# Optimization experiments

Hardware: AMD Instinct MI355X
Metric: run time of the kernel (lower is better)

Reference implementation:

```python
import jax, jax.numpy as jnp
import numpy as np

SIGMA = 1.0
DELTA = 1.0
TOPK = 10
TOPK_HALF = int(np.around(TOPK / 2))  # 5
EPS = 1e-12


def _cdist(a, b):
    # Euclidean distance matrix, grad-safe sqrt at zero (matches torch.cdist values).
    d2 = (jnp.sum(a * a, axis=1)[:, None]
          + jnp.sum(b * b, axis=1)[None, :]
          - 2.0 * (a @ b.T))
    d2 = jnp.maximum(d2, 0.0)
    pos = d2 > 0.0
    return jnp.where(pos, jnp.sqrt(jnp.where(pos, d2, 1.0)), 0.0)


def _consistency_weights(t_emb):
    # Everything here is under torch.no_grad() in the original.
    N = t_emb.shape[0]
    T_dist = _cdist(t_emb, t_emb)
    W_P = jnp.exp(-(T_dist ** 2) / SIGMA)
    _, idx = jax.lax.top_k(W_P, TOPK)                      # [N, TOPK]
    rows = jnp.arange(N)[:, None]
    W_NN = jnp.zeros_like(W_P).at[rows, idx].set(1.0)      # scatter_ ones
    V = (((W_NN + W_NN.T) / 2) == 1.0).astype(W_P.dtype)   # mutual kNN (symmetric)
    # Vectorized form of the per-row python loop:
    #   W_C_tilda[i, j] = V[i, j] * (sum_k V[i, k] * V[j, k]) / sum_k V[i, k]
    deg = jnp.sum(V, axis=1)                               # >= 1 (self is always a NN)
    overlap = V @ V.T                                      # [N, N] neighbor overlap
    W_C_tilda = V * overlap / deg[:, None]
    topk_half_index = idx[:, :TOPK_HALF]                   # [N, TOPK_HALF]
    W_C_hat = jnp.mean(W_C_tilda[topk_half_index], axis=1) # gather rows, mean -> [N, N]
    W_C = (W_C_hat + W_C_hat.T) / 2
    return (W_P + W_C) / 2


def reference(s_emb, t_emb):
    # disable_mu = 0 -> s_emb NOT normalized; t_emb always normalized.
    t_norm = t_emb / jnp.maximum(
        jnp.linalg.norm(t_emb, axis=1, keepdims=True), EPS)
    N = s_emb.shape[0]
    S_dist = _cdist(s_emb, s_emb)
    S_dist = S_dist / jnp.mean(S_dist, axis=1, keepdims=True)
    W = jax.lax.stop_gradient(_consistency_weights(t_norm))
    off_diag = 1.0 - jnp.eye(N, dtype=W.dtype)
    pos_weight = W * off_diag
    neg_weight = (1.0 - W) * off_diag
    pull = jnp.maximum(S_dist, 0.0) ** 2 * pos_weight
    push = jnp.maximum(DELTA - S_dist, 0.0) ** 2 * neg_weight
    return (jnp.sum(pull) + jnp.sum(push)) / (N * (N - 1))


def setup_inputs() -> dict:
    key = jax.random.key(0)
    k1, k2 = jax.random.split(key)
    N, D = 2048, 1024
    return {
        "s_emb": jax.random.normal(k1, (N, D), dtype=jnp.float32),
        "t_emb": jax.random.normal(k2, (N, D), dtype=jnp.float32),
    }
```

## Files before the change

### kernel.cpp

```cpp
#include <hip/hip_runtime.h>
#include <math.h>

#define N_ 2048
#define D_ 1024
#define TOPK 10
#define TOPK_HALF 5
#define INV_NORM (1.0f / ((float)N_ * (float)(N_ - 1)))

typedef __attribute__((ext_vector_type(8))) short short8;
typedef __attribute__((ext_vector_type(4))) float floatx4;

__device__ __forceinline__ short f2bf(float f) {
  unsigned u = __float_as_uint(f);
  unsigned r = (u + 0x7fffu + ((u >> 16) & 1u)) >> 16;
  return (short)r;
}
__device__ __forceinline__ float bf2f(short b) {
  return __uint_as_float(((unsigned)(unsigned short)b) << 16);
}

__device__ __forceinline__ void gld_lds16(const short* g, short* l) {
  __builtin_amdgcn_global_load_lds(
      (const __attribute__((address_space(1))) unsigned int*)(g),
      (__attribute__((address_space(3))) unsigned int*)(l), 16, 0, 0);
}

#define BAR() asm volatile("s_barrier" ::: "memory")
#define WAIT8_BAR() asm volatile("s_waitcnt vmcnt(8)\ns_barrier" ::: "memory")
#define WAIT0_BAR() asm volatile("s_waitcnt vmcnt(0)\ns_barrier" ::: "memory")

__global__ __launch_bounds__(256) void prep_kernel(const float* __restrict__ t,
                                                   const float* __restrict__ s,
                                                   short* __restrict__ tb,
                                                   short* __restrict__ sb,
                                                   float* __restrict__ tt,
                                                   float* __restrict__ ss,
                                                   float* __restrict__ rowsum,
                                                   float* __restrict__ out) {
  int b = blockIdx.x, tid = threadIdx.x;
  __shared__ float red[256];
  if (b == 0) {
    for (int j = tid; j < N_; j += 256) rowsum[j] = 0.f;
    if (tid == 0) out[0] = 0.f;
  }
  if (b < N_) {
    const float* rp = t + (size_t)b * D_;
    short* op = tb + (size_t)b * D_;
    float acc = 0.f;
    for (int k = tid; k < D_; k += 256) { float v = rp[k]; acc += v * v; }
    red[tid] = acc; __syncthreads();
    for (int st = 128; st > 0; st >>= 1) { if (tid < st) red[tid] += red[tid + st]; __syncthreads(); }
    float denom = fmaxf(sqrtf(red[0]), 1e-12f);
    __syncthreads();
    float s2 = 0.f;
    for (int k = tid; k < D_; k += 256) { float v = rp[k] / denom; op[k] = f2bf(v); s2 += v * v; }
    red[tid] = s2; __syncthreads();
    for (int st = 128; st > 0; st >>= 1) { if (tid < st) red[tid] += red[tid + st]; __syncthreads(); }
    if (tid == 0) tt[b] = red[0];
  } else {
    int row = b - N_;
    const float* rp = s + (size_t)row * D_;
    short* op = sb + (size_t)row * D_;
    float acc = 0.f;
    for (int k = tid; k < D_; k += 256) { float v = rp[k]; op[k] = f2bf(v); acc += v * v; }
    red[tid] = acc; __syncthreads();
    for (int st = 128; st > 0; st >>= 1) { if (tid < st) red[tid] += red[tid + st]; __syncthreads(); }
    if (tid == 0) ss[row] = red[0];
  }
}

__global__ __launch_bounds__(256) void gram_mfma_kernel(
    const short* __restrict__ Tb, const short* __restrict__ Sb,
    const float* __restrict__ tt, const float* __restrict__ ss,
    short* __restrict__ WPb, short* __restrict__ Sob,
    float* __restrict__ rowsum) {
  const int mode = blockIdx.z;
  const short* A = mode ? Sb : Tb;
  const float* rn = mode ? ss : tt;
  short* outb = mode ? Sob : WPb;

  __shared__ __align__(16) short As[2][128 * 64];
  __shared__ __align__(16) short Bs[2][128 * 64];

  int tid = threadIdx.x;
  int w = tid >> 6, lane = tid & 63;
  int i0 = blockIdx.y * 128, j0 = blockIdx.x * 128;
  int wr = w >> 1, wc = w & 1;
  int quad = lane >> 4, l16 = lane & 15;

  floatx4 acc[4][4] = {};

  int srow = w * 32 + (lane >> 3);
  int gchunk = ((lane & 7) ^ (lane >> 3)) * 8;
  const short* Ag = A + (size_t)(i0 + srow) * D_ + gchunk;
  const short* Bg = A + (size_t)(j0 + srow) * D_ + gchunk;
  int sloc = srow * 64 + (lane & 7) * 8;

#define STAGE(buf, k0)                                        \
  do {                                                        \
    _Pragma("unroll") for (int q = 0; q < 4; q++) {           \
      gld_lds16(Ag + (k0) + (size_t)q * 8 * D_, &As[buf][sloc + q * 8 * 64]); \
      gld_lds16(Bg + (k0) + (size_t)q * 8 * D_, &Bs[buf][sloc + q * 8 * 64]); \
    }                                                         \
  } while (0)

  STAGE(0, 0);
#pragma unroll 2
  for (int it = 0; it < 16; it++) {
    int cur = it & 1;
    if (it) BAR();
    if (it < 15) {
      STAGE(!cur, (it + 1) * 64);
      WAIT8_BAR();
    } else {
      WAIT0_BAR();
    }
    const short* Ab = As[cur];
    const short* Bb = Bs[cur];
#pragma unroll
    for (int ks = 0; ks < 64; ks += 32) {
      int cb = ks >> 3;
      short8 af[4], bfr[4];
#pragma unroll
      for (int mt = 0; mt < 4; mt++) {
        int r = wr * 64 + mt * 16 + l16;
        af[mt] = *(const short8*)&Ab[r * 64 + (((cb + quad) ^ (l16 & 7)) << 3)];
      }
#pragma unroll
      for (int nt = 0; nt < 4; nt++) {
        int r = wc * 64 + nt * 16 + l16;
        bfr[nt] = *(const short8*)&Bb[r * 64 + (((cb + quad) ^ (l16 & 7)) << 3)];
      }
#pragma unroll
      for (int mt = 0; mt < 4; mt++)
#pragma unroll
        for (int nt = 0; nt < 4; nt++)
          acc[mt][nt] = __builtin_amdgcn_mfma_f32_16x16x32_bf16(af[mt], bfr[nt], acc[mt][nt], 0, 0, 0);
    }
  }

#pragma unroll
  for (int mt = 0; mt < 4; mt++) {
#pragma unroll
    for (int r = 0; r < 4; r++) {
      int i = i0 + wr * 64 + mt * 16 + quad * 4 + r;
      float ri = rn[i];
      float rs = 0.f;
#pragma unroll
      for (int nt = 0; nt < 4; nt++) {
        int j = j0 + wc * 64 + nt * 16 + l16;
        float d2 = fmaxf(ri + rn[j] - 2.f * acc[mt][nt][r], 0.f);
        float o = mode ? sqrtf(d2) : expf(-d2);
        if (i == j) o = mode ? 0.f : 1.f;
        outb[(size_t)i * N_ + j] = f2bf(o);
        rs += o;
      }
      if (mode) {
        rs += __shfl_xor(rs, 1); rs += __shfl_xor(rs, 2);
        rs += __shfl_xor(rs, 4); rs += __shfl_xor(rs, 8);
        if (l16 == 0) atomicAdd(&rowsum[i], rs);
      }
    }
  }
}

__global__ __launch_bounds__(64) void topk_loss_kernel(const short* __restrict__ WPb,
                                                       const short* __restrict__ Sb,
                                                       const float* __restrict__ rowsum,
                                                       int* __restrict__ idx,
                                                       unsigned* __restrict__ mask,
                                                       float* __restrict__ out) {
  int row = blockIdx.x, lane = threadIdx.x;
  const short8* wpr = (const short8*)(WPb + (size_t)row * N_);
  const short8* sr = (const short8*)(Sb + (size_t)row * N_);
  float rminv = (float)N_ / rowsum[row];
  float w[32];
  float local = 0.f;
#pragma unroll
  for (int c4 = 0; c4 < 4; c4++) {
    short8 wp8 = wpr[lane * 4 + c4];
    short8 s8 = sr[lane * 4 + c4];
#pragma unroll
    for (int e = 0; e < 8; e++) {
      float wv = bf2f(wp8[e]);
      w[c4 * 8 + e] = wv;
      float sv = bf2f(s8[e]) * rminv;
      float d = fmaxf(1.f - sv, 0.f);
      local += d * d + 0.5f * wv * (sv * sv - d * d);
    }
  }
#pragma unroll
  for (int off = 32; off > 0; off >>= 1) local += __shfl_down(local, off);
  if (lane == 0) {
    atomicAdd(out, (local - 0.5f) * INV_NORM);
    mask[row] = 0u;
  }
  int base = lane * 32;
  int sel[TOPK];
  for (int t = 0; t < TOPK; t++) {
    float bv = -2.f; int bi = 0;
#pragma unroll
    for (int c = 0; c < 32; c++)
      if (w[c] > bv) { bv = w[c]; bi = base + c; }
#pragma unroll
    for (int off = 32; off > 0; off >>= 1) {
      float ov = __shfl_down(bv, off);
      int oi = __shfl_down(bi, off);
      if (ov > bv || (ov == bv && oi < bi)) { bv = ov; bi = oi; }
    }
    bi = __shfl(bi, 0);
    sel[t] = bi;
    bool mine = (bi >> 5) == lane;
    int cc = bi & 31;
#pragma unroll
    for (int c = 0; c < 32; c++)
      if (mine && cc == c) w[c] = -1.f;
  }
  if (lane == 0) {
#pragma unroll
    for (int t = 0; t < TOPK; t++) idx[row * TOPK + t] = sel[t];
  }
}

__global__ __launch_bounds__(256) void mutual_kernel(const int* __restrict__ idx,
                                                     unsigned* __restrict__ mask) {
  int t = blockIdx.x * 256 + threadIdx.x;
  int i = t >> 4, k = t & 15;
  if (i >= N_ || k >= TOPK) return;
  int j = idx[i * TOPK + k];
  bool mut = false;
#pragma unroll
  for (int l = 0; l < TOPK; l++) mut |= (idx[j * TOPK + l] == i);
  if (mut) atomicOr(&mask[i], 1u << k);
}

__global__ __launch_bounds__(256) void sparse_wc_kernel(
    const int* __restrict__ idx, const unsigned* __restrict__ mask,
    const short* __restrict__ Sb, const float* __restrict__ rowsum,
    float* __restrict__ out) {
  int t = blockIdx.x * 256 + threadIdx.x;
  int i = t >> 6, r = t & 63;
  float contrib = 0.f;
  if (i < N_ && r < TOPK_HALF * TOPK) {
    int mi = r / TOPK, k = r - mi * TOPK;
    int m = idx[i * TOPK + mi];
    unsigned mm = mask[m];
    if ((mm >> k) & 1u) {
      int col = idx[m * TOPK + k];
      if (col != i) {
        int dm = __popc(mm);
        unsigned mc = mask[col];
        int jm[TOPK], jc[TOPK];
#pragma unroll
        for (int l = 0; l < TOPK; l++) jm[l] = idx[m * TOPK + l];
#pragma unroll
        for (int l = 0; l < TOPK; l++) jc[l] = idx[col * TOPK + l];
        int c = 0;
#pragma unroll
        for (int a = 0; a < TOPK; a++) {
          if ((mm >> a) & 1u) {
            int na = jm[a];
#pragma unroll
            for (int b = 0; b < TOPK; b++) c += (((mc >> b) & 1u) && (jc[b] == na));
          }
        }
        float v = (float)c / (float)dm * 0.1f;
        float s1 = bf2f(Sb[(size_t)i * N_ + col]) * ((float)N_ / rowsum[i]);
        float d1 = fmaxf(1.f - s1, 0.f);
        float s2 = bf2f(Sb[(size_t)col * N_ + i]) * ((float)N_ / rowsum[col]);
        float d2 = fmaxf(1.f - s2, 0.f);
        contrib = 0.5f * v * ((s1 * s1 - d1 * d1) + (s2 * s2 - d2 * d2));
      }
    }
  }
  __shared__ float red[256];
  red[threadIdx.x] = contrib; __syncthreads();
  for (int st = 128; st > 0; st >>= 1) {
    if (threadIdx.x < st) red[threadIdx.x] += red[threadIdx.x + st];
    __syncthreads();
  }
  if (threadIdx.x == 0) atomicAdd(out, red[0] * INV_NORM);
}

extern "C" void kernel_launch(void* const* d_in, const int* in_sizes, int n_in,
                              void* d_out, int out_size, void* d_ws, size_t ws_size,
                              hipStream_t stream) {
  const float* s_emb = (const float*)d_in[0];
  const float* t_emb = (const float*)d_in[1];
  float* out = (float*)d_out;

  const size_t NN = (size_t)N_ * N_;
  const size_t ND = (size_t)N_ * D_;
  short* t_bf = (short*)d_ws;
  short* s_bf = t_bf + ND;
  short* WPb = s_bf + ND;
  short* Sb = WPb + NN;
  float* tt = (float*)(Sb + NN);
  float* ss = tt + N_;
  float* rowsum = ss + N_;
  int* idx = (int*)(rowsum + N_);
  unsigned* mask = (unsigned*)(idx + (size_t)N_ * TOPK);

  prep_kernel<<<2 * N_, 256, 0, stream>>>(t_emb, s_emb, t_bf, s_bf, tt, ss, rowsum, out);

  dim3 g(N_ / 128, N_ / 128, 2);
  gram_mfma_kernel<<<g, 256, 0, stream>>>(t_bf, s_bf, tt, ss, WPb, Sb, rowsum);

  topk_loss_kernel<<<N_, 64, 0, stream>>>(WPb, Sb, rowsum, idx, mask, out);
  mutual_kernel<<<N_ * 16 / 256, 256, 0, stream>>>(idx, mask);
  sparse_wc_kernel<<<N_ * 64 / 256, 256, 0, stream>>>(idx, mask, Sb, rowsum, out);
}
```

Baseline: 149.7 us.

## Exploit Gram symmetry with 64x64 triangular tiles and vectorize prep kernel

The Gram kernel now computes only lower-triangular 64x64 tiles (528 per matrix) and writes each off-diagonal tile's transpose through LDS, also adding column sums to rowsum for the S distance matrix. This roughly halves the MFMA work, at the cost of smaller tiles with less register reuse, extra transposed stores and more atomics. The prep kernel is rewritten to load each row once as float4 and store packed bf16 pairs, removing the second global read of t.

```diff
diff --git a/kernel.cpp b/kernel.cpp
--- a/kernel.cpp
+++ b/kernel.cpp
@@ -26,7 +26,7 @@
 }
 
 #define BAR() asm volatile("s_barrier" ::: "memory")
-#define WAIT8_BAR() asm volatile("s_waitcnt vmcnt(8)\ns_barrier" ::: "memory")
+#define WAIT4_BAR() asm volatile("s_waitcnt vmcnt(4)\ns_barrier" ::: "memory")
 #define WAIT0_BAR() asm volatile("s_waitcnt vmcnt(0)\ns_barrier" ::: "memory")
 
 __global__ __launch_bounds__(256) void prep_kernel(const float* __restrict__ t,
@@ -44,64 +44,80 @@
     if (tid == 0) out[0] = 0.f;
   }
   if (b < N_) {
-    const float* rp = t + (size_t)b * D_;
-    short* op = tb + (size_t)b * D_;
-    float acc = 0.f;
-    for (int k = tid; k < D_; k += 256) { float v = rp[k]; acc += v * v; }
-    red[tid] = acc; __syncthreads();
+    const float4* rp = (const float4*)(t + (size_t)b * D_);
+    float4 v = rp[tid];
+    red[tid] = v.x * v.x + v.y * v.y + v.z * v.z + v.w * v.w;
+    __syncthreads();
     for (int st = 128; st > 0; st >>= 1) { if (tid < st) red[tid] += red[tid + st]; __syncthreads(); }
-    float denom = fmaxf(sqrtf(red[0]), 1e-12f);
-    __syncthreads();
-    float s2 = 0.f;
-    for (int k = tid; k < D_; k += 256) { float v = rp[k] / denom; op[k] = f2bf(v); s2 += v * v; }
-    red[tid] = s2; __syncthreads();
+    float inv = 1.f / fmaxf(sqrtf(red[0]), 1e-12f);
+    __syncthreads();
+    float a = v.x * inv, bb = v.y * inv, c = v.z * inv, d = v.w * inv;
+    uint2 pk;
+    pk.x = (unsigned)(unsigned short)f2bf(a) | ((unsigned)(unsigned short)f2bf(bb) << 16);
+    pk.y = (unsigned)(unsigned short)f2bf(c) | ((unsigned)(unsigned short)f2bf(d) << 16);
+    ((uint2*)(tb + (size_t)b * D_))[tid] = pk;
+    red[tid] = a * a + bb * bb + c * c + d * d;
+    __syncthreads();
     for (int st = 128; st > 0; st >>= 1) { if (tid < st) red[tid] += red[tid + st]; __syncthreads(); }
     if (tid == 0) tt[b] = red[0];
   } else {
     int row = b - N_;
-    const float* rp = s + (size_t)row * D_;
-    short* op = sb + (size_t)row * D_;
-    float acc = 0.f;
-    for (int k = tid; k < D_; k += 256) { float v = rp[k]; op[k] = f2bf(v); acc += v * v; }
-    red[tid] = acc; __syncthreads();
+    const float4* rp = (const float4*)(s + (size_t)row * D_);
+    float4 v = rp[tid];
+    uint2 pk;
+    pk.x = (unsigned)(unsigned short)f2bf(v.x) | ((unsigned)(unsigned short)f2bf(v.y) << 16);
+    pk.y = (unsigned)(unsigned short)f2bf(v.z) | ((unsigned)(unsigned short)f2bf(v.w) << 16);
+    ((uint2*)(sb + (size_t)row * D_))[tid] = pk;
+    red[tid] = v.x * v.x + v.y * v.y + v.z * v.z + v.w * v.w;
+    __syncthreads();
     for (int st = 128; st > 0; st >>= 1) { if (tid < st) red[tid] += red[tid + st]; __syncthreads(); }
     if (tid == 0) ss[row] = red[0];
   }
 }
 
-__global__ __launch_bounds__(256) void gram_mfma_kernel(
+#define NTRI 528
+__global__ __launch_bounds__(256) void gram_sym_kernel(
     const short* __restrict__ Tb, const short* __restrict__ Sb,
     const float* __restrict__ tt, const float* __restrict__ ss,
     short* __restrict__ WPb, short* __restrict__ Sob,
     float* __restrict__ rowsum) {
-  const int mode = blockIdx.z;
+  int p = blockIdx.x;
+  const int mode = (p >= NTRI);
+  int q = p - mode * NTRI;
+  int bi = (int)((sqrtf(8.f * (float)q + 1.f) - 1.f) * 0.5f);
+  if (bi > 31) bi = 31;
+  while ((bi + 1) * (bi + 2) / 2 <= q) bi++;
+  while (bi * (bi + 1) / 2 > q) bi--;
+  int bj = q - bi * (bi + 1) / 2;
+
   const short* A = mode ? Sb : Tb;
   const float* rn = mode ? ss : tt;
   short* outb = mode ? Sob : WPb;
 
-  __shared__ __align__(16) short As[2][128 * 64];
-  __shared__ __align__(16) short Bs[2][128 * 64];
+  __shared__ __align__(16) short smem[4 * 4096];
 
   int tid = threadIdx.x;
   int w = tid >> 6, lane = tid & 63;
-  int i0 = blockIdx.y * 128, j0 = blockIdx.x * 128;
+  int i0 = bi * 64, j0 = bj * 64;
   int wr = w >> 1, wc = w & 1;
   int quad = lane >> 4, l16 = lane & 15;
 
-  floatx4 acc[4][4] = {};
-
-  int srow = w * 32 + (lane >> 3);
-  int gchunk = ((lane & 7) ^ (lane >> 3)) * 8;
-  const short* Ag = A + (size_t)(i0 + srow) * D_ + gchunk;
-  const short* Bg = A + (size_t)(j0 + srow) * D_ + gchunk;
-  int sloc = srow * 64 + (lane & 7) * 8;
-
-#define STAGE(buf, k0)                                        \
-  do {                                                        \
-    _Pragma("unroll") for (int q = 0; q < 4; q++) {           \
-      gld_lds16(Ag + (k0) + (size_t)q * 8 * D_, &As[buf][sloc + q * 8 * 64]); \
-      gld_lds16(Bg + (k0) + (size_t)q * 8 * D_, &Bs[buf][sloc + q * 8 * 64]); \
-    }                                                         \
+  floatx4 acc[2][2] = {};
+
+  int sr8 = lane >> 3;
+  int gch = ((lane & 7) ^ sr8) * 8;
+  const short* Ag = A + (size_t)(i0 + w * 16 + sr8) * D_ + gch;
+  const short* Bg = A + (size_t)(j0 + w * 16 + sr8) * D_ + gch;
+  int lloc = (w * 16 + sr8) * 64 + (lane & 7) * 8;
+
+#define STAGE(buf, k0)                                                   \
+  do {                                                                   \
+    short* Al = smem + (buf)*8192 + lloc;                                \
+    short* Bl = smem + (buf)*8192 + 4096 + lloc;                         \
+    gld_lds16(Ag + (k0), Al);                                            \
+    gld_lds16(Ag + (k0) + (size_t)8 * D_, Al + 512);                     \
+    gld_lds16(Bg + (k0), Bl);                                            \
+    gld_lds16(Bg + (k0) + (size_t)8 * D_, Bl + 512);                     \
   } while (0)
 
   STAGE(0, 0);
@@ -111,47 +127,49 @@
     if (it) BAR();
     if (it < 15) {
       STAGE(!cur, (it + 1) * 64);
-      WAIT8_BAR();
+      WAIT4_BAR();
     } else {
       WAIT0_BAR();
     }
-    const short* Ab = As[cur];
-    const short* Bb = Bs[cur];
+    const short* Ab = smem + cur * 8192;
+    const short* Bb = smem + cur * 8192 + 4096;
 #pragma unroll
     for (int ks = 0; ks < 64; ks += 32) {
       int cb = ks >> 3;
-      short8 af[4], bfr[4];
-#pragma unroll
-      for (int mt = 0; mt < 4; mt++) {
-        int r = wr * 64 + mt * 16 + l16;
-        af[mt] = *(const short8*)&Ab[r * 64 + (((cb + quad) ^ (l16 & 7)) << 3)];
-      }
-#pragma unroll
-      for (int nt = 0; nt < 4; nt++) {
-        int r = wc * 64 + nt * 16 + l16;
-        bfr[nt] = *(const short8*)&Bb[r * 64 + (((cb + quad) ^ (l16 & 7)) << 3)];
-      }
-#pragma unroll
-      for (int mt = 0; mt < 4; mt++)
-#pragma unroll
-        for (int nt = 0; nt < 4; nt++)
+      short8 af[2], bfr[2];
+#pragma unroll
+      for (int mt = 0; mt < 2; mt++) {
+        int rr = wr * 32 + mt * 16 + l16;
+        af[mt] = *(const short8*)&Ab[rr * 64 + (((cb + quad) ^ (l16 & 7)) << 3)];
+      }
+#pragma unroll
+      for (int nt = 0; nt < 2; nt++) {
+        int rr = wc * 32 + nt * 16 + l16;
+        bfr[nt] = *(const short8*)&Bb[rr * 64 + (((cb + quad) ^ (l16 & 7)) << 3)];
+      }
+#pragma unroll
+      for (int mt = 0; mt < 2; mt++)
+#pragma unroll
+        for (int nt = 0; nt < 2; nt++)
           acc[mt][nt] = __builtin_amdgcn_mfma_f32_16x16x32_bf16(af[mt], bfr[nt], acc[mt][nt], 0, 0, 0);
     }
   }
 
-#pragma unroll
-  for (int mt = 0; mt < 4; mt++) {
+  float ov[2][2][4];
+#pragma unroll
+  for (int mt = 0; mt < 2; mt++) {
 #pragma unroll
     for (int r = 0; r < 4; r++) {
-      int i = i0 + wr * 64 + mt * 16 + quad * 4 + r;
+      int i = i0 + wr * 32 + mt * 16 + quad * 4 + r;
       float ri = rn[i];
       float rs = 0.f;
 #pragma unroll
-      for (int nt = 0; nt < 4; nt++) {
-        int j = j0 + wc * 64 + nt * 16 + l16;
+      for (int nt = 0; nt < 2; nt++) {
+        int j = j0 + wc * 32 + nt * 16 + l16;
         float d2 = fmaxf(ri + rn[j] - 2.f * acc[mt][nt][r], 0.f);
         float o = mode ? sqrtf(d2) : expf(-d2);
         if (i == j) o = mode ? 0.f : 1.f;
+        ov[mt][nt][r] = o;
         outb[(size_t)i * N_ + j] = f2bf(o);
         rs += o;
       }
@@ -160,6 +178,46 @@
         rs += __shfl_xor(rs, 4); rs += __shfl_xor(rs, 8);
         if (l16 == 0) atomicAdd(&rowsum[i], rs);
       }
+    }
+  }
+
+  if (bi != bj) {
+    if (mode) {
+#pragma unroll
+      for (int nt = 0; nt < 2; nt++) {
+        float cs = 0.f;
+#pragma unroll
+        for (int mt = 0; mt < 2; mt++)
+#pragma unroll
+          for (int r = 0; r < 4; r++) cs += ov[mt][nt][r];
+        cs += __shfl_xor(cs, 16);
+        cs += __shfl_xor(cs, 32);
+        if (quad == 0) atomicAdd(&rowsum[j0 + wc * 32 + nt * 16 + l16], cs);
+      }
+    }
+    BAR();
+    float* fs = (float*)smem + w * 1088;
+#pragma unroll
+    for (int mt = 0; mt < 2; mt++)
+#pragma unroll
+      for (int nt = 0; nt < 2; nt++)
+#pragma unroll
+        for (int r = 0; r < 4; r++) {
+          int lr = mt * 16 + quad * 4 + r;
+          int lc = nt * 16 + l16;
+          fs[lc * 34 + lr] = ov[mt][nt][r];
+        }
+#pragma unroll
+    for (int itx = 0; itx < 8; itx++) {
+      int sidx = itx * 64 + lane;
+      int lc = sidx >> 4;
+      int k2 = (sidx & 15) * 2;
+      float lo = fs[lc * 34 + k2];
+      float hi = fs[lc * 34 + k2 + 1];
+      unsigned pk = (unsigned)(unsigned short)f2bf(lo) |
+                    ((unsigned)(unsigned short)f2bf(hi) << 16);
+      size_t jg = (size_t)(j0 + wc * 32 + lc);
+      *(unsigned*)(outb + jg * N_ + i0 + wr * 32 + k2) = pk;
     }
   }
 }
@@ -204,9 +262,9 @@
       if (w[c] > bv) { bv = w[c]; bi = base + c; }
 #pragma unroll
     for (int off = 32; off > 0; off >>= 1) {
-      float ov = __shfl_down(bv, off);
+      float ovv = __shfl_down(bv, off);
       int oi = __shfl_down(bi, off);
-      if (ov > bv || (ov == bv && oi < bi)) { bv = ov; bi = oi; }
+      if (ovv > bv || (ovv == bv && oi < bi)) { bv = ovv; bi = oi; }
     }
     bi = __shfl(bi, 0);
     sel[t] = bi;
@@ -303,8 +361,7 @@
 
   prep_kernel<<<2 * N_, 256, 0, stream>>>(t_emb, s_emb, t_bf, s_bf, tt, ss, rowsum, out);
 
-  dim3 g(N_ / 128, N_ / 128, 2);
-  gram_mfma_kernel<<<g, 256, 0, stream>>>(t_bf, s_bf, tt, ss, WPb, Sb, rowsum);
+  gram_sym_kernel<<<2 * NTRI, 256, 0, stream>>>(t_bf, s_bf, tt, ss, WPb, Sb, rowsum);
 
   topk_loss_kernel<<<N_, 64, 0, stream>>>(WPb, Sb, rowsum, idx, mask, out);
   mutual_kernel<<<N_ * 16 / 256, 256, 0, stream>>>(idx, mask);
```

Measured after the change: 141.3 us. 5.6% less time.
